# Performance work log

Hardware: AMD Instinct MI355X
Metric: run time of the kernel (lower is better)

Reference implementation:

```python
import jax, jax.numpy as jnp
import numpy as np

N = 50000      # nodes
E = 800000     # edges
DIN = 128
DH = 128
DE = 128
DOUT = 2
EPS = 1e-5     # GraphNorm eps


def _xavier(key, fan_in, fan_out):
    lim = float(np.sqrt(6.0 / (fan_in + fan_out)))
    return jax.random.uniform(key, (fan_in, fan_out), jnp.float32, -lim, lim)


def setup_inputs() -> dict:
    key = jax.random.key(0)
    ks = jax.random.split(key, 8)
    x = jax.random.normal(ks[0], (N, DIN), jnp.float32)
    edge_index = jax.random.randint(ks[1], (2, E), 0, N, dtype=jnp.int32)
    W1 = _xavier(ks[2], DIN, DH); b1 = jnp.zeros((DH,), jnp.float32)
    W2 = _xavier(ks[3], DH, DH);  b2 = jnp.zeros((DH,), jnp.float32)
    W3 = _xavier(ks[4], DH, DE);  b3 = jnp.zeros((DE,), jnp.float32)
    gn1_w = jnp.ones((DH,), jnp.float32); gn1_b = jnp.zeros((DH,), jnp.float32); gn1_a = jnp.ones((DH,), jnp.float32)
    gn2_w = jnp.ones((DH,), jnp.float32); gn2_b = jnp.zeros((DH,), jnp.float32); gn2_a = jnp.ones((DH,), jnp.float32)
    Wout = _xavier(ks[5], DE, DOUT); bout = jnp.zeros((DOUT,), jnp.float32)
    return {
        "x": x, "edge_index": edge_index,
        "W1": W1, "b1": b1, "W2": W2, "b2": b2, "W3": W3, "b3": b3,
        "gn1_w": gn1_w, "gn1_b": gn1_b, "gn1_a": gn1_a,
        "gn2_w": gn2_w, "gn2_b": gn2_b, "gn2_a": gn2_a,
        "Wout": Wout, "bout": bout,
    }


def gcn_conv(x, src, dst, W, b):
    # PyG GCNConv: add self-loops, symmetric normalization, linear, scatter-add at dst.
    n = x.shape[0]
    h = x @ W                                   # [N, C]
    loop = jnp.arange(n, dtype=src.dtype)
    s = jnp.concatenate([src, loop])            # [E+N]
    d = jnp.concatenate([dst, loop])
    deg = jnp.zeros((n,), h.dtype).at[d].add(1.0)
    dinv = jnp.where(deg > 0, jax.lax.rsqrt(deg), 0.0)
    norm = dinv[s] * dinv[d]                    # [E+N]
    out = jnp.zeros_like(h).at[d].add(h[s] * norm[:, None])
    return out + b


def graph_norm(h, w, b, alpha):
    # Single-graph GraphNorm: shift by alpha*mean, normalize by variance of shifted values.
    mean = h.mean(axis=0)
    c = h - alpha * mean
    var = (c * c).mean(axis=0)
    return c * jax.lax.rsqrt(var + EPS) * w + b


def reference(x, edge_index, W1, b1, W2, b2, W3, b3,
              gn1_w, gn1_b, gn1_a, gn2_w, gn2_b, gn2_a, Wout, bout):
    src, dst = edge_index[0], edge_index[1]
    h = gcn_conv(x, src, dst, W1, b1)
    h = jax.nn.relu(graph_norm(h, gn1_w, gn1_b, gn1_a))   # dropout identity (eval)
    h = gcn_conv(h, src, dst, W2, b2)
    h = jax.nn.relu(graph_norm(h, gn2_w, gn2_b, gn2_a))
    h = gcn_conv(h, src, dst, W3, b3)
    return h @ Wout + bout
```

## Files before the change

kernel.cpp:

```cpp
#include <hip/hip_runtime.h>
#include <hip/hip_bf16.h>

#define GN_EPS 1e-5f


typedef __attribute__((ext_vector_type(8))) short short8;
typedef __attribute__((ext_vector_type(4))) float f32x4;

__device__ __forceinline__ unsigned short f2bf(float f) {
    unsigned u = __float_as_uint(f);
    u += 0x7fffu + ((u >> 16) & 1u);
    return (unsigned short)(u >> 16);
}
__device__ __forceinline__ float bflo(unsigned u) { return __uint_as_float(u << 16); }
__device__ __forceinline__ float bfhi(unsigned u) { return __uint_as_float(u & 0xffff0000u); }

__global__ void k_degi(const int* __restrict__ dst, int* __restrict__ degi,
                       unsigned short* __restrict__ slot, int e) {
    int i = blockIdx.x * blockDim.x + threadIdx.x;
    if (i < e) slot[i] = (unsigned short)atomicAdd(&degi[dst[i]], 1);
}

#define SCAN_CHUNK 4096
__global__ __launch_bounds__(256) void k_blocksum(const int* __restrict__ degi,
                                                  int* __restrict__ partial, int n) {
    int base = blockIdx.x * SCAN_CHUNK + threadIdx.x * 16;
    int s = 0;
    #pragma unroll
    for (int q = 0; q < 16; ++q) {
        int i = base + q;
        if (i < n) s += degi[i];
    }
    #pragma unroll
    for (int off = 32; off; off >>= 1) s += __shfl_down(s, off);
    __shared__ int ws[4];
    if ((threadIdx.x & 63) == 0) ws[threadIdx.x >> 6] = s;
    __syncthreads();
    if (threadIdx.x == 0) partial[blockIdx.x] = ws[0] + ws[1] + ws[2] + ws[3];
}

__global__ __launch_bounds__(256) void k_scanfinal(const int* __restrict__ degi,
                                                   const int* __restrict__ partial,
                                                   int* __restrict__ rowptr,
                                                   float* __restrict__ dinv, int n, int nb) {
    int blockbase = 0;
    for (int i = 0; i < (int)blockIdx.x; ++i) blockbase += partial[i];

    int base = blockIdx.x * SCAN_CHUNK + threadIdx.x * 16;
    int v[16];
    int s = 0;
    #pragma unroll
    for (int q = 0; q < 16; ++q) {
        int i = base + q;
        v[q] = (i < n) ? degi[i] : 0;
        s += v[q];
    }
    const int lane = threadIdx.x & 63;
    const int wid = threadIdx.x >> 6;
    int x = s;
    #pragma unroll
    for (int off = 1; off < 64; off <<= 1) {
        int t = __shfl_up(x, off);
        if (lane >= off) x += t;
    }
    __shared__ int ws[4];
    if (lane == 63) ws[wid] = x;
    __syncthreads();
    int waveoff = 0;
    if (wid > 0) waveoff += ws[0];
    if (wid > 1) waveoff += ws[1];
    if (wid > 2) waveoff += ws[2];
    int excl = x - s + waveoff + blockbase;
    #pragma unroll
    for (int q = 0; q < 16; ++q) {
        int i = base + q;
        if (i < n) {
            rowptr[i] = excl;
            dinv[i] = rsqrtf((float)(v[q] + 1));
        }
        excl += v[q];
    }
    if ((int)blockIdx.x == nb - 1 && threadIdx.x == 255) {
        rowptr[n] = excl;
    }
}

__global__ void k_fill(const int* __restrict__ src, const int* __restrict__ dst,
                       const unsigned short* __restrict__ slot, const int* __restrict__ rowptr,
                       const float* __restrict__ dinv,
                       unsigned* __restrict__ csr_ew, int e) {
    int i = blockIdx.x * blockDim.x + threadIdx.x;
    if (i < e) {
        int s = src[i], d = dst[i];
        float w = dinv[s] * dinv[d];
        csr_ew[rowptr[d] + (int)slot[i]] = ((unsigned)s << 16) | (unsigned)f2bf(w);
    }
}

__global__ __launch_bounds__(256) void k_prepW2(const float* __restrict__ W1,
                                                const float* __restrict__ W2,
                                                unsigned short* __restrict__ Wt) {
    const float* W = blockIdx.x == 0 ? W1 : W2;
    unsigned short* o = Wt + blockIdx.x * 16384;
    __shared__ unsigned short sT[128 * 130];
    const float4* W4 = (const float4*)W;
    for (int idx = threadIdx.x; idx < 128 * 32; idx += 256) {
        int k = idx >> 5, c4 = idx & 31;
        float4 v = W4[k * 32 + c4];
        sT[(c4 * 4 + 0) * 130 + k] = f2bf(v.x);
        sT[(c4 * 4 + 1) * 130 + k] = f2bf(v.y);
        sT[(c4 * 4 + 2) * 130 + k] = f2bf(v.z);
        sT[(c4 * 4 + 3) * 130 + k] = f2bf(v.w);
    }
    __syncthreads();
    for (int idx = threadIdx.x; idx < 128 * 128; idx += 256) {
        int c = idx >> 7, k = idx & 127;
        o[idx] = sT[c * 130 + k];
    }
}

__global__ __launch_bounds__(128) void k_prepM(const float* __restrict__ W3,
                                               const float* __restrict__ Wo,
                                               const float* __restrict__ b3,
                                               const float* __restrict__ bo,
                                               float* __restrict__ M,
                                               float* __restrict__ mb) {
    int k = threadIdx.x;
    float m0 = 0.f, m1 = 0.f;
    for (int c = 0; c < 128; ++c) {
        float w = W3[k * 128 + c];
        m0 += w * Wo[c * 2];
        m1 += w * Wo[c * 2 + 1];
    }
    M[k * 2] = m0;
    M[k * 2 + 1] = m1;
    if (k < 2) {
        float s = 0.f;
        for (int c = 0; c < 128; ++c) s += b3[c] * Wo[c * 2 + k];
        mb[k] = s + bo[k];
    }
}

#define LDK 136
__global__ __launch_bounds__(256) void k_gemm_f32(const float* __restrict__ X,
                                                  const unsigned short* __restrict__ Wt,
                                                  unsigned short* __restrict__ Y,
                                                  int nrows) {
    __shared__ __align__(16) unsigned short sX[64 * LDK];
    __shared__ __align__(16) unsigned short sB[128 * LDK];
    const int t = threadIdx.x;
    const int row0 = blockIdx.x * 64;

    for (int idx = t; idx < 128 * 16; idx += 256) {
        int c = idx >> 4, ch = idx & 15;
        uint4 v = ((const uint4*)(Wt + c * 128))[ch];
        *(uint4*)(&sB[c * LDK + ch * 8]) = v;
    }
    for (int idx = t; idx < 64 * 32; idx += 256) {
        int r = idx >> 5, c4 = idx & 31;
        int grow = row0 + r;
        float4 v = make_float4(0.f, 0.f, 0.f, 0.f);
        if (grow < nrows) v = ((const float4*)(X + (size_t)grow * 128))[c4];
        ushort4 o;
        o.x = f2bf(v.x); o.y = f2bf(v.y); o.z = f2bf(v.z); o.w = f2bf(v.w);
        *(ushort4*)(&sX[r * LDK + c4 * 4]) = o;
    }
    __syncthreads();

    const int w = t >> 6;
    const int lane = t & 63;
    const int m = lane & 15;
    const int quad = lane >> 4;

    f32x4 acc[8] = {};
    #pragma unroll
    for (int ks = 0; ks < 4; ++ks) {
        int ko = ks * 32 + quad * 8;
        short8 a = *(const short8*)(&sX[(w * 16 + m) * LDK + ko]);
        #pragma unroll
        for (int ct = 0; ct < 8; ++ct) {
            short8 b = *(const short8*)(&sB[(ct * 16 + m) * LDK + ko]);
            acc[ct] = __builtin_amdgcn_mfma_f32_16x16x32_bf16(a, b, acc[ct], 0, 0, 0);
        }
    }
    #pragma unroll
    for (int r = 0; r < 4; ++r) {
        int grow = row0 + w * 16 + quad * 4 + r;
        if (grow >= nrows) continue;
        unsigned short* yr = Y + (size_t)grow * 128 + m;
        #pragma unroll
        for (int ct = 0; ct < 8; ++ct) yr[ct * 16] = f2bf(acc[ct][r]);
    }
}

__global__ __launch_bounds__(256) void k_gemm_bf(const unsigned short* __restrict__ Xb,
                                                 const unsigned short* __restrict__ Wt,
                                                 unsigned short* __restrict__ Y,
                                                 const float* __restrict__ cs,
                                                 const float* __restrict__ cb,
                                                 int nrows) {
    __shared__ __align__(16) unsigned short sX[64 * LDK];
    __shared__ __align__(16) unsigned short sB[128 * LDK];
    const int t = threadIdx.x;
    const int row0 = blockIdx.x * 64;

    for (int idx = t; idx < 128 * 16; idx += 256) {
        int c = idx >> 4, ch = idx & 15;
        uint4 v = ((const uint4*)(Wt + c * 128))[ch];
        *(uint4*)(&sB[c * LDK + ch * 8]) = v;
    }
    for (int idx = t; idx < 64 * 32; idx += 256) {
        int r = idx >> 5, c4 = idx & 31;
        int grow = row0 + r;
        uint2 u = make_uint2(0u, 0u);
        if (grow < nrows) u = *(const uint2*)(Xb + (size_t)grow * 128 + c4 * 4);
        float4 s4 = ((const float4*)cs)[c4];
        float4 b4 = ((const float4*)cb)[c4];
        ushort4 o;
        o.x = f2bf(fmaxf(fmaf(bflo(u.x), s4.x, b4.x), 0.f));
        o.y = f2bf(fmaxf(fmaf(bfhi(u.x), s4.y, b4.y), 0.f));
        o.z = f2bf(fmaxf(fmaf(bflo(u.y), s4.z, b4.z), 0.f));
        o.w = f2bf(fmaxf(fmaf(bfhi(u.y), s4.w, b4.w), 0.f));
        *(ushort4*)(&sX[r * LDK + c4 * 4]) = o;
    }
    __syncthreads();

    const int w = t >> 6;
    const int lane = t & 63;
    const int m = lane & 15;
    const int quad = lane >> 4;

    f32x4 acc[8] = {};
    #pragma unroll
    for (int ks = 0; ks < 4; ++ks) {
        int ko = ks * 32 + quad * 8;
        short8 a = *(const short8*)(&sX[(w * 16 + m) * LDK + ko]);
        #pragma unroll
        for (int ct = 0; ct < 8; ++ct) {
            short8 b = *(const short8*)(&sB[(ct * 16 + m) * LDK + ko]);
            acc[ct] = __builtin_amdgcn_mfma_f32_16x16x32_bf16(a, b, acc[ct], 0, 0, 0);
        }
    }
    #pragma unroll
    for (int r = 0; r < 4; ++r) {
        int grow = row0 + w * 16 + quad * 4 + r;
        if (grow >= nrows) continue;
        unsigned short* yr = Y + (size_t)grow * 128 + m;
        #pragma unroll
        for (int ct = 0; ct < 8; ++ct) yr[ct * 16] = f2bf(acc[ct][r]);
    }
}

__global__ __launch_bounds__(256) void k_gather(const unsigned short* __restrict__ H,
                                                unsigned short* __restrict__ O,
                                                const int* __restrict__ rowptr,
                                                const unsigned* __restrict__ csr_ew,
                                                const float* __restrict__ dinv,
                                                const float* __restrict__ bias, int n) {
    int node = blockIdx.x * 4 + (threadIdx.x >> 6);
    if (node >= n) return;
    int lane = threadIdx.x & 63;
    int qw = lane >> 4;
    int ql = lane & 15;
    const uint4* Hx = (const uint4*)H;
    float di = dinv[node];
    float acc[8] = {};
    if (qw == 0) {
        uint4 u = Hx[(size_t)node * 16 + ql];
        float dd = di * di;
        float4 ba = ((const float4*)bias)[ql * 2];
        float4 bb = ((const float4*)bias)[ql * 2 + 1];
        acc[0] = bflo(u.x) * dd + ba.x; acc[1] = bfhi(u.x) * dd + ba.y;
        acc[2] = bflo(u.y) * dd + ba.z; acc[3] = bfhi(u.y) * dd + ba.w;
        acc[4] = bflo(u.z) * dd + bb.x; acc[5] = bfhi(u.z) * dd + bb.y;
        acc[6] = bflo(u.w) * dd + bb.z; acc[7] = bfhi(u.w) * dd + bb.w;
    }
    int j = rowptr[node];
    const int end = rowptr[node + 1];
    for (; j + 15 < end; j += 16) {
        unsigned ew[4];
        #pragma unroll
        for (int q = 0; q < 4; ++q) ew[q] = csr_ew[j + 4 * q + qw];
        uint4 u[4];
        #pragma unroll
        for (int q = 0; q < 4; ++q) u[q] = Hx[(size_t)(ew[q] >> 16) * 16 + ql];
        #pragma unroll
        for (int q = 0; q < 4; ++q) {
            float nr = __uint_as_float(ew[q] << 16);
            acc[0] += bflo(u[q].x) * nr; acc[1] += bfhi(u[q].x) * nr;
            acc[2] += bflo(u[q].y) * nr; acc[3] += bfhi(u[q].y) * nr;
            acc[4] += bflo(u[q].z) * nr; acc[5] += bfhi(u[q].z) * nr;
            acc[6] += bflo(u[q].w) * nr; acc[7] += bfhi(u[q].w) * nr;
        }
    }
    for (int jj = j + qw; jj < end; jj += 4) {
        unsigned ew = csr_ew[jj];
        uint4 u = Hx[(size_t)(ew >> 16) * 16 + ql];
        float nr = __uint_as_float(ew << 16);
        acc[0] += bflo(u.x) * nr; acc[1] += bfhi(u.x) * nr;
        acc[2] += bflo(u.y) * nr; acc[3] += bfhi(u.y) * nr;
        acc[4] += bflo(u.z) * nr; acc[5] += bfhi(u.z) * nr;
        acc[6] += bflo(u.w) * nr; acc[7] += bfhi(u.w) * nr;
    }
    #pragma unroll
    for (int i = 0; i < 8; ++i) {
        acc[i] += __shfl_down(acc[i], 32);
        acc[i] += __shfl_down(acc[i], 16);
    }
    if (qw == 0) {
        uint4 o;
        o.x = (unsigned)f2bf(acc[0]) | ((unsigned)f2bf(acc[1]) << 16);
        o.y = (unsigned)f2bf(acc[2]) | ((unsigned)f2bf(acc[3]) << 16);
        o.z = (unsigned)f2bf(acc[4]) | ((unsigned)f2bf(acc[5]) << 16);
        o.w = (unsigned)f2bf(acc[6]) | ((unsigned)f2bf(acc[7]) << 16);
        *(uint4*)(O + (size_t)node * 128 + ql * 8) = o;
    }
}

__global__ __launch_bounds__(256) void k_zproj(const unsigned short* __restrict__ Xb,
                                               const float* __restrict__ M,
                                               const float* __restrict__ cs,
                                               const float* __restrict__ cb,
                                               float2* __restrict__ Z, int n) {
    int node = blockIdx.x * 4 + (threadIdx.x >> 6);
    if (node >= n) return;
    int lane = threadIdx.x & 63;
    unsigned u = ((const unsigned*)Xb)[(size_t)node * 64 + lane];
    int c0 = lane * 2;
    float a = fmaxf(fmaf(bflo(u), cs[c0], cb[c0]), 0.f);
    float b = fmaxf(fmaf(bfhi(u), cs[c0 + 1], cb[c0 + 1]), 0.f);
    float p0 = a * M[c0 * 2]     + b * M[(c0 + 1) * 2];
    float p1 = a * M[c0 * 2 + 1] + b * M[(c0 + 1) * 2 + 1];
    #pragma unroll
    for (int off = 32; off; off >>= 1) {
        p0 += __shfl_down(p0, off);
        p1 += __shfl_down(p1, off);
    }
    if (lane == 0) Z[node] = make_float2(p0, p1);
}

__global__ __launch_bounds__(256) void k_gatherZ(const float2* __restrict__ Z,
                                                 const int* __restrict__ rowptr,
                                                 const unsigned* __restrict__ csr_ew,
                                                 const float* __restrict__ dinv,
                                                 const float* __restrict__ mb,
                                                 float* __restrict__ out, int n) {
    int wid = threadIdx.x >> 6;
    int lane = threadIdx.x & 63;
    int g = lane >> 4;
    int gl = lane & 15;
    int node = blockIdx.x * 16 + wid * 4 + g;
    if (node >= n) return;
    float2 acc = make_float2(0.f, 0.f);
    if (gl == 0) {
        float di = dinv[node];
        float2 z = Z[node];
        acc.x = z.x * di * di + mb[0];
        acc.y = z.y * di * di + mb[1];
    }
    int j = rowptr[node];
    const int end = rowptr[node + 1];
    for (int jj = j + gl; jj < end; jj += 16) {
        unsigned ew = csr_ew[jj];
        float2 z = Z[ew >> 16];
        float w = __uint_as_float(ew << 16);
        acc.x += z.x * w;
        acc.y += z.y * w;
    }
    #pragma unroll
    for (int off = 8; off; off >>= 1) {
        acc.x += __shfl_down(acc.x, off);
        acc.y += __shfl_down(acc.y, off);
    }
    if (gl == 0) {
        out[(size_t)node * 2]     = acc.x;
        out[(size_t)node * 2 + 1] = acc.y;
    }
}

#define STAT_NB 256
__global__ __launch_bounds__(256) void k_stats(const unsigned short* __restrict__ H,
                                               float* __restrict__ pS,
                                               float* __restrict__ pQ, int n) {
    const uint4* H4 = (const uint4*)H;
    const size_t nv = (size_t)n * 16;
    float s[8] = {}, q[8] = {};
    for (size_t f = (size_t)blockIdx.x * 256 + threadIdx.x; f < nv;
         f += (size_t)256 * STAT_NB) {
        uint4 u = H4[f];
        float v;
        v = bflo(u.x); s[0] += v; q[0] += v * v;
        v = bfhi(u.x); s[1] += v; q[1] += v * v;
        v = bflo(u.y); s[2] += v; q[2] += v * v;
        v = bfhi(u.y); s[3] += v; q[3] += v * v;
        v = bflo(u.z); s[4] += v; q[4] += v * v;
        v = bfhi(u.z); s[5] += v; q[5] += v * v;
        v = bflo(u.w); s[6] += v; q[6] += v * v;
        v = bfhi(u.w); s[7] += v; q[7] += v * v;
    }
    __shared__ float ls[256][9], lq[256][9];
    int t = threadIdx.x;
    #pragma unroll
    for (int i = 0; i < 8; ++i) { ls[t][i] = s[i]; lq[t][i] = q[i]; }
    __syncthreads();
    #pragma unroll
    for (int off = 128; off >= 16; off >>= 1) {
        if (t < off) {
            #pragma unroll
            for (int i = 0; i < 8; ++i) { ls[t][i] += ls[t + off][i]; lq[t][i] += lq[t + off][i]; }
        }
        __syncthreads();
    }
    if (t < 16) {
        #pragma unroll
        for (int i = 0; i < 8; ++i) {
            pS[(size_t)blockIdx.x * 128 + t * 8 + i] = ls[t][i];
            pQ[(size_t)blockIdx.x * 128 + t * 8 + i] = lq[t][i];
        }
    }
}

__global__ void k_finstats(const float* __restrict__ pS, const float* __restrict__ pQ,
                           const float* __restrict__ w, const float* __restrict__ b,
                           const float* __restrict__ alpha,
                           float* __restrict__ colscale, float* __restrict__ colshift,
                           int n) {
    int c = threadIdx.x;
    if (c >= 128) return;
    float s = 0.f, q = 0.f;
    #pragma unroll 8
    for (int blk = 0; blk < STAT_NB; ++blk) {
        s += pS[blk * 128 + c];
        q += pQ[blk * 128 + c];
    }
    float inv_n = 1.0f / (float)n;
    float m = s * inv_n;
    float eh2 = q * inv_n;
    float a = alpha[c];
    float var = eh2 - (2.0f * a - a * a) * m * m;
    float scale = rsqrtf(var + GN_EPS) * w[c];
    colscale[c] = scale;
    colshift[c] = b[c] - a * m * scale;
}

extern "C" void kernel_launch(void* const* d_in, const int* in_sizes, int n_in,
                              void* d_out, int out_size, void* d_ws, size_t ws_size,
                              hipStream_t stream) {
    const float* x    = (const float*)d_in[0];
    const int*   ei   = (const int*)  d_in[1];
    const float* W1   = (const float*)d_in[2];
    const float* b1   = (const float*)d_in[3];
    const float* W2   = (const float*)d_in[4];
    const float* b2   = (const float*)d_in[5];
    const float* W3   = (const float*)d_in[6];
    const float* b3   = (const float*)d_in[7];
    const float* gn1w = (const float*)d_in[8];
    const float* gn1b = (const float*)d_in[9];
    const float* gn1a = (const float*)d_in[10];
    const float* gn2w = (const float*)d_in[11];
    const float* gn2b = (const float*)d_in[12];
    const float* gn2a = (const float*)d_in[13];
    const float* Wout = (const float*)d_in[14];
    const float* bout = (const float*)d_in[15];
    float* out = (float*)d_out;

    const int n = in_sizes[0] / 128;
    const int e = in_sizes[1] / 2;
    const int* srcI = ei;
    const int* dstI = ei + e;

    unsigned short* bufH = (unsigned short*)d_ws;
    unsigned short* bufG = bufH + (size_t)n * 128;
    unsigned short* slot = bufH;
    float* dinv     = (float*)(bufG + (size_t)n * 128);
    float* colscale = dinv + n;
    float* colshift = colscale + 128;
    int*   degi     = (int*)(colshift + 128);
    int*   rowptr   = degi + n;
    int*   partial  = rowptr + n + 1;
    float* pS       = (float*)(partial + 64);
    float* pQ       = pS + STAT_NB * 128;
    unsigned* csr_ew = (unsigned*)(pQ + STAT_NB * 128);
    unsigned short* Wt = (unsigned short*)(csr_ew + e);
    float* M        = (float*)(Wt + 2 * 16384);
    float* mb       = M + 256;
    float2* Z       = (float2*)(mb + 2);

    const int nb = (n + SCAN_CHUNK - 1) / SCAN_CHUNK;

    hipMemsetAsync(degi, 0, (size_t)n * sizeof(int), stream);
    k_degi<<<(e + 255) / 256, 256, 0, stream>>>(dstI, degi, slot, e);
    k_blocksum<<<nb, 256, 0, stream>>>(degi, partial, n);
    k_scanfinal<<<nb, 256, 0, stream>>>(degi, partial, rowptr, dinv, n, nb);
    k_fill<<<(e + 255) / 256, 256, 0, stream>>>(srcI, dstI, slot, rowptr, dinv, csr_ew, e);
    k_prepW2<<<2, 256, 0, stream>>>(W1, W2, Wt);
    k_prepM<<<1, 128, 0, stream>>>(W3, Wout, b3, bout, M, mb);

    const int gemmGrid = (n + 63) / 64;
    const int gathGrid = (n + 3) / 4;

    k_gemm_f32<<<gemmGrid, 256, 0, stream>>>(x, Wt, bufH, n);
    k_gather<<<gathGrid, 256, 0, stream>>>(bufH, bufG, rowptr, csr_ew, dinv, b1, n);
    k_stats<<<STAT_NB, 256, 0, stream>>>(bufG, pS, pQ, n);
    k_finstats<<<1, 128, 0, stream>>>(pS, pQ, gn1w, gn1b, gn1a, colscale, colshift, n);

    k_gemm_bf<<<gemmGrid, 256, 0, stream>>>(bufG, Wt + 16384, bufH, colscale, colshift, n);
    k_gather<<<gathGrid, 256, 0, stream>>>(bufH, bufG, rowptr, csr_ew, dinv, b2, n);
    k_stats<<<STAT_NB, 256, 0, stream>>>(bufG, pS, pQ, n);
    k_finstats<<<1, 128, 0, stream>>>(pS, pQ, gn2w, gn2b, gn2a, colscale, colshift, n);

    k_zproj<<<gathGrid, 256, 0, stream>>>(bufG, M, colscale, colshift, Z, n);
    k_gatherZ<<<(n + 15) / 16, 256, 0, stream>>>(Z, rowptr, csr_ew, dinv, mb, out, n);
}
```

Baseline: 317.2 us.

## Pad CSR rows to 16 and fuse GraphNorm stats into gather

```diff
diff --git a/kernel.cpp b/kernel.cpp
--- a/kernel.cpp
+++ b/kernel.cpp
@@ -1,5 +1,4 @@
 #include <hip/hip_runtime.h>
-#include <hip/hip_bf16.h>
 
 #define GN_EPS 1e-5f
 
@@ -29,7 +28,7 @@
     #pragma unroll
     for (int q = 0; q < 16; ++q) {
         int i = base + q;
-        if (i < n) s += degi[i];
+        if (i < n) s += (degi[i] + 15) & ~15;
     }
     #pragma unroll
     for (int off = 32; off; off >>= 1) s += __shfl_down(s, off);
@@ -47,13 +46,14 @@
     for (int i = 0; i < (int)blockIdx.x; ++i) blockbase += partial[i];
 
     int base = blockIdx.x * SCAN_CHUNK + threadIdx.x * 16;
-    int v[16];
+    int v[16], pv[16];
     int s = 0;
     #pragma unroll
     for (int q = 0; q < 16; ++q) {
         int i = base + q;
         v[q] = (i < n) ? degi[i] : 0;
-        s += v[q];
+        pv[q] = (v[q] + 15) & ~15;
+        s += pv[q];
     }
     const int lane = threadIdx.x & 63;
     const int wid = threadIdx.x >> 6;
@@ -78,7 +78,7 @@
             rowptr[i] = excl;
             dinv[i] = rsqrtf((float)(v[q] + 1));
         }
-        excl += v[q];
+        excl += pv[q];
     }
     if ((int)blockIdx.x == nb - 1 && threadIdx.x == 255) {
         rowptr[n] = excl;
@@ -97,47 +97,50 @@
     }
 }
 
-__global__ __launch_bounds__(256) void k_prepW2(const float* __restrict__ W1,
-                                                const float* __restrict__ W2,
-                                                unsigned short* __restrict__ Wt) {
-    const float* W = blockIdx.x == 0 ? W1 : W2;
-    unsigned short* o = Wt + blockIdx.x * 16384;
+__global__ __launch_bounds__(256) void k_prep(const float* __restrict__ W1,
+                                              const float* __restrict__ W2,
+                                              const float* __restrict__ W3,
+                                              const float* __restrict__ Wo,
+                                              const float* __restrict__ b3,
+                                              const float* __restrict__ bo,
+                                              unsigned short* __restrict__ Wt,
+                                              float* __restrict__ M,
+                                              float* __restrict__ mb) {
     __shared__ unsigned short sT[128 * 130];
-    const float4* W4 = (const float4*)W;
-    for (int idx = threadIdx.x; idx < 128 * 32; idx += 256) {
-        int k = idx >> 5, c4 = idx & 31;
-        float4 v = W4[k * 32 + c4];
-        sT[(c4 * 4 + 0) * 130 + k] = f2bf(v.x);
-        sT[(c4 * 4 + 1) * 130 + k] = f2bf(v.y);
-        sT[(c4 * 4 + 2) * 130 + k] = f2bf(v.z);
-        sT[(c4 * 4 + 3) * 130 + k] = f2bf(v.w);
-    }
-    __syncthreads();
-    for (int idx = threadIdx.x; idx < 128 * 128; idx += 256) {
-        int c = idx >> 7, k = idx & 127;
-        o[idx] = sT[c * 130 + k];
-    }
-}
-
-__global__ __launch_bounds__(128) void k_prepM(const float* __restrict__ W3,
-                                               const float* __restrict__ Wo,
-                                               const float* __restrict__ b3,
-                                               const float* __restrict__ bo,
-                                               float* __restrict__ M,
-                                               float* __restrict__ mb) {
-    int k = threadIdx.x;
-    float m0 = 0.f, m1 = 0.f;
-    for (int c = 0; c < 128; ++c) {
-        float w = W3[k * 128 + c];
-        m0 += w * Wo[c * 2];
-        m1 += w * Wo[c * 2 + 1];
-    }
-    M[k * 2] = m0;
-    M[k * 2 + 1] = m1;
-    if (k < 2) {
-        float s = 0.f;
-        for (int c = 0; c < 128; ++c) s += b3[c] * Wo[c * 2 + k];
-        mb[k] = s + bo[k];
+    if (blockIdx.x < 2) {
+        const float* W = blockIdx.x == 0 ? W1 : W2;
+        unsigned short* o = Wt + blockIdx.x * 16384;
+        const float4* W4 = (const float4*)W;
+        for (int idx = threadIdx.x; idx < 128 * 32; idx += 256) {
+            int k = idx >> 5, c4 = idx & 31;
+            float4 v = W4[k * 32 + c4];
+            sT[(c4 * 4 + 0) * 130 + k] = f2bf(v.x);
+            sT[(c4 * 4 + 1) * 130 + k] = f2bf(v.y);
+            sT[(c4 * 4 + 2) * 130 + k] = f2bf(v.z);
+            sT[(c4 * 4 + 3) * 130 + k] = f2bf(v.w);
+        }
+        __syncthreads();
+        for (int idx = threadIdx.x; idx < 128 * 128; idx += 256) {
+            int c = idx >> 7, k = idx & 127;
+            o[idx] = sT[c * 130 + k];
+        }
+    } else {
+        int k = threadIdx.x;
+        if (k < 128) {
+            float m0 = 0.f, m1 = 0.f;
+            for (int c = 0; c < 128; ++c) {
+                float w = W3[k * 128 + c];
+                m0 += w * Wo[c * 2];
+                m1 += w * Wo[c * 2 + 1];
+            }
+            M[k * 2] = m0;
+            M[k * 2 + 1] = m1;
+            if (k < 2) {
+                float s = 0.f;
+                for (int c = 0; c < 128; ++c) s += b3[c] * Wo[c * 2 + k];
+                mb[k] = s + bo[k];
+            }
+        }
     }
 }
 
@@ -256,64 +259,90 @@
                                                 const int* __restrict__ rowptr,
                                                 const unsigned* __restrict__ csr_ew,
                                                 const float* __restrict__ dinv,
-                                                const float* __restrict__ bias, int n) {
-    int node = blockIdx.x * 4 + (threadIdx.x >> 6);
-    if (node >= n) return;
-    int lane = threadIdx.x & 63;
-    int qw = lane >> 4;
-    int ql = lane & 15;
+                                                const float* __restrict__ bias,
+                                                float* __restrict__ pS,
+                                                float* __restrict__ pQ, int n) {
+    __shared__ float sS[4][128];
+    __shared__ float sQ[4][128];
+    const int wid = threadIdx.x >> 6;
+    const int node = blockIdx.x * 4 + wid;
+    const int lane = threadIdx.x & 63;
+    const int qw = lane >> 4;
+    const int ql = lane & 15;
     const uint4* Hx = (const uint4*)H;
-    float di = dinv[node];
     float acc[8] = {};
+    if (node < n) {
+        float di = dinv[node];
+        if (qw == 0) {
+            uint4 u = Hx[(size_t)node * 16 + ql];
+            float dd = di * di;
+            float4 ba = ((const float4*)bias)[ql * 2];
+            float4 bb = ((const float4*)bias)[ql * 2 + 1];
+            acc[0] = bflo(u.x) * dd + ba.x; acc[1] = bfhi(u.x) * dd + ba.y;
+            acc[2] = bflo(u.y) * dd + ba.z; acc[3] = bfhi(u.y) * dd + ba.w;
+            acc[4] = bflo(u.z) * dd + bb.x; acc[5] = bfhi(u.z) * dd + bb.y;
+            acc[6] = bflo(u.w) * dd + bb.z; acc[7] = bfhi(u.w) * dd + bb.w;
+        }
+        int j = rowptr[node];
+        const int end = rowptr[node + 1];
+        for (; j < end; j += 16) {
+            unsigned ew[4];
+            #pragma unroll
+            for (int q = 0; q < 4; ++q) ew[q] = csr_ew[j + 4 * q + qw];
+            uint4 u[4];
+            #pragma unroll
+            for (int q = 0; q < 4; ++q) {
+                unsigned idx = ((ew[q] >> 12) & 0xFFFF0u) + (unsigned)ql;
+                u[q] = Hx[idx];
+            }
+            #pragma unroll
+            for (int q = 0; q < 4; ++q) {
+                float nr = __uint_as_float(ew[q] << 16);
+                acc[0] += bflo(u[q].x) * nr; acc[1] += bfhi(u[q].x) * nr;
+                acc[2] += bflo(u[q].y) * nr; acc[3] += bfhi(u[q].y) * nr;
+                acc[4] += bflo(u[q].z) * nr; acc[5] += bfhi(u[q].z) * nr;
+                acc[6] += bflo(u[q].w) * nr; acc[7] += bfhi(u[q].w) * nr;
+            }
+        }
+        #pragma unroll
+        for (int i = 0; i < 8; ++i) {
+            acc[i] += __shfl_down(acc[i], 32);
+            acc[i] += __shfl_down(acc[i], 16);
+        }
+    }
     if (qw == 0) {
-        uint4 u = Hx[(size_t)node * 16 + ql];
-        float dd = di * di;
-        float4 ba = ((const float4*)bias)[ql * 2];
-        float4 bb = ((const float4*)bias)[ql * 2 + 1];
-        acc[0] = bflo(u.x) * dd + ba.x; acc[1] = bfhi(u.x) * dd + ba.y;
-        acc[2] = bflo(u.y) * dd + ba.z; acc[3] = bfhi(u.y) * dd + ba.w;
-        acc[4] = bflo(u.z) * dd + bb.x; acc[5] = bfhi(u.z) * dd + bb.y;
-        acc[6] = bflo(u.w) * dd + bb.z; acc[7] = bfhi(u.w) * dd + bb.w;
-    }
-    int j = rowptr[node];
-    const int end = rowptr[node + 1];
-    for (; j + 15 < end; j += 16) {
-        unsigned ew[4];
-        #pragma unroll
-        for (int q = 0; q < 4; ++q) ew[q] = csr_ew[j + 4 * q + qw];
-        uint4 u[4];
-        #pragma unroll
-        for (int q = 0; q < 4; ++q) u[q] = Hx[(size_t)(ew[q] >> 16) * 16 + ql];
-        #pragma unroll
-        for (int q = 0; q < 4; ++q) {
-            float nr = __uint_as_float(ew[q] << 16);
-            acc[0] += bflo(u[q].x) * nr; acc[1] += bfhi(u[q].x) * nr;
-            acc[2] += bflo(u[q].y) * nr; acc[3] += bfhi(u[q].y) * nr;
-            acc[4] += bflo(u[q].z) * nr; acc[5] += bfhi(u[q].z) * nr;
-            acc[6] += bflo(u[q].w) * nr; acc[7] += bfhi(u[q].w) * nr;
-        }
-    }
-    for (int jj = j + qw; jj < end; jj += 4) {
-        unsigned ew = csr_ew[jj];
-        uint4 u = Hx[(size_t)(ew >> 16) * 16 + ql];
-        float nr = __uint_as_float(ew << 16);
-        acc[0] += bflo(u.x) * nr; acc[1] += bfhi(u.x) * nr;
-        acc[2] += bflo(u.y) * nr; acc[3] += bfhi(u.y) * nr;
-        acc[4] += bflo(u.z) * nr; acc[5] += bfhi(u.z) * nr;
-        acc[6] += bflo(u.w) * nr; acc[7] += bfhi(u.w) * nr;
-    }
-    #pragma unroll
-    for (int i = 0; i < 8; ++i) {
-        acc[i] += __shfl_down(acc[i], 32);
-        acc[i] += __shfl_down(acc[i], 16);
-    }
-    if (qw == 0) {
-        uint4 o;
-        o.x = (unsigned)f2bf(acc[0]) | ((unsigned)f2bf(acc[1]) << 16);
-        o.y = (unsigned)f2bf(acc[2]) | ((unsigned)f2bf(acc[3]) << 16);
-        o.z = (unsigned)f2bf(acc[4]) | ((unsigned)f2bf(acc[5]) << 16);
-        o.w = (unsigned)f2bf(acc[6]) | ((unsigned)f2bf(acc[7]) << 16);
-        *(uint4*)(O + (size_t)node * 128 + ql * 8) = o;
+        if (node < n) {
+            unsigned short h[8];
+            float v[8];
+            #pragma unroll
+            for (int i = 0; i < 8; ++i) {
+                h[i] = f2bf(acc[i]);
+                v[i] = __uint_as_float((unsigned)h[i] << 16);
+                sS[wid][ql * 8 + i] = v[i];
+                sQ[wid][ql * 8 + i] = v[i] * v[i];
+            }
+            uint4 o;
+            o.x = (unsigned)h[0] | ((unsigned)h[1] << 16);
+            o.y = (unsigned)h[2] | ((unsigned)h[3] << 16);
+            o.z = (unsigned)h[4] | ((unsigned)h[5] << 16);
+            o.w = (unsigned)h[6] | ((unsigned)h[7] << 16);
+            *(uint4*)(O + (size_t)node * 128 + ql * 8) = o;
+        } else {
+            #pragma unroll
+            for (int i = 0; i < 8; ++i) {
+                sS[wid][ql * 8 + i] = 0.f;
+                sQ[wid][ql * 8 + i] = 0.f;
+            }
+        }
+    }
+    __syncthreads();
+    const int t = threadIdx.x;
+    if (t < 128) {
+        float s = sS[0][t] + sS[1][t] + sS[2][t] + sS[3][t];
+        float q = sQ[0][t] + sQ[1][t] + sQ[2][t] + sQ[3][t];
+        const int slotb = (blockIdx.x & 63) << 7;
+        atomicAdd(&pS[slotb + t], s);
+        atomicAdd(&pQ[slotb + t], q);
     }
 }
 
@@ -378,48 +407,6 @@
     }
 }
 
-#define STAT_NB 256
-__global__ __launch_bounds__(256) void k_stats(const unsigned short* __restrict__ H,
-                                               float* __restrict__ pS,
-                                               float* __restrict__ pQ, int n) {
-    const uint4* H4 = (const uint4*)H;
-    const size_t nv = (size_t)n * 16;
-    float s[8] = {}, q[8] = {};
-    for (size_t f = (size_t)blockIdx.x * 256 + threadIdx.x; f < nv;
-         f += (size_t)256 * STAT_NB) {
-        uint4 u = H4[f];
-        float v;
-        v = bflo(u.x); s[0] += v; q[0] += v * v;
-        v = bfhi(u.x); s[1] += v; q[1] += v * v;
-        v = bflo(u.y); s[2] += v; q[2] += v * v;
-        v = bfhi(u.y); s[3] += v; q[3] += v * v;
-        v = bflo(u.z); s[4] += v; q[4] += v * v;
-        v = bfhi(u.z); s[5] += v; q[5] += v * v;
-        v = bflo(u.w); s[6] += v; q[6] += v * v;
-        v = bfhi(u.w); s[7] += v; q[7] += v * v;
-    }
-    __shared__ float ls[256][9], lq[256][9];
-    int t = threadIdx.x;
-    #pragma unroll
-    for (int i = 0; i < 8; ++i) { ls[t][i] = s[i]; lq[t][i] = q[i]; }
-    __syncthreads();
-    #pragma unroll
-    for (int off = 128; off >= 16; off >>= 1) {
-        if (t < off) {
-            #pragma unroll
-            for (int i = 0; i < 8; ++i) { ls[t][i] += ls[t + off][i]; lq[t][i] += lq[t + off][i]; }
-        }
-        __syncthreads();
-    }
-    if (t < 16) {
-        #pragma unroll
-        for (int i = 0; i < 8; ++i) {
-            pS[(size_t)blockIdx.x * 128 + t * 8 + i] = ls[t][i];
-            pQ[(size_t)blockIdx.x * 128 + t * 8 + i] = lq[t][i];
-        }
-    }
-}
-
 __global__ void k_finstats(const float* __restrict__ pS, const float* __restrict__ pQ,
                            const float* __restrict__ w, const float* __restrict__ b,
                            const float* __restrict__ alpha,
@@ -429,7 +416,7 @@
     if (c >= 128) return;
     float s = 0.f, q = 0.f;
     #pragma unroll 8
-    for (int blk = 0; blk < STAT_NB; ++blk) {
+    for (int blk = 0; blk < 64; ++blk) {
         s += pS[blk * 128 + c];
         q += pQ[blk * 128 + c];
     }
@@ -469,45 +456,54 @@
     const int* srcI = ei;
     const int* dstI = ei + e;
 
-    unsigned short* bufH = (unsigned short*)d_ws;
-    unsigned short* bufG = bufH + (size_t)n * 128;
+    char* base = (char*)d_ws;
+    size_t off = 0;
+    auto take = [&](size_t bytes) -> void* {
+        void* r = base + off;
+        off += (bytes + 15) & ~(size_t)15;
+        return r;
+    };
+    unsigned short* bufH = (unsigned short*)take((size_t)n * 256);
+    unsigned short* bufG = (unsigned short*)take((size_t)n * 256);
+    float* dinv     = (float*)take((size_t)n * 4);
+    float* colscale = (float*)take(128 * 4);
+    float* colshift = (float*)take(128 * 4);
+    int*   rowptr   = (int*)take(((size_t)n + 1) * 4);
+    int*   partial  = (int*)take(64 * 4);
+    unsigned short* Wt = (unsigned short*)take(2 * 16384 * 2);
+    float* M        = (float*)take(256 * 4);
+    float* mb       = (float*)take(2 * 4);
+    float2* Z       = (float2*)take((size_t)n * 8);
+    int*   degi     = (int*)take((size_t)n * 4);
+    float* pS       = (float*)take(2 * 64 * 128 * 4);
+    float* pQ       = (float*)take(2 * 64 * 128 * 4);
+    size_t csr_cap  = (size_t)e + 16 * (size_t)n;
+    unsigned* csr_ew = (unsigned*)take(csr_cap * 4);
+    size_t zbytes   = (size_t)((base + off) - (char*)degi);
+
     unsigned short* slot = bufH;
-    float* dinv     = (float*)(bufG + (size_t)n * 128);
-    float* colscale = dinv + n;
-    float* colshift = colscale + 128;
-    int*   degi     = (int*)(colshift + 128);
-    int*   rowptr   = degi + n;
-    int*   partial  = rowptr + n + 1;
-    float* pS       = (float*)(partial + 64);
-    float* pQ       = pS + STAT_NB * 128;
-    unsigned* csr_ew = (unsigned*)(pQ + STAT_NB * 128);
-    unsigned short* Wt = (unsigned short*)(csr_ew + e);
-    float* M        = (float*)(Wt + 2 * 16384);
-    float* mb       = M + 256;
-    float2* Z       = (float2*)(mb + 2);
 
     const int nb = (n + SCAN_CHUNK - 1) / SCAN_CHUNK;
 
-    hipMemsetAsync(degi, 0, (size_t)n * sizeof(int), stream);
+    hipMemsetAsync(degi, 0, zbytes, stream);
     k_degi<<<(e + 255) / 256, 256, 0, stream>>>(dstI, degi, slot, e);
     k_blocksum<<<nb, 256, 0, stream>>>(degi, partial, n);
     k_scanfinal<<<nb, 256, 0, stream>>>(degi, partial, rowptr, dinv, n, nb);
     k_fill<<<(e + 255) / 256, 256, 0, stream>>>(srcI, dstI, slot, rowptr, dinv, csr_ew, e);
-    k_prepW2<<<2, 256, 0, stream>>>(W1, W2, Wt);
-    k_prepM<<<1, 128, 0, stream>>>(W3, Wout, b3, bout, M, mb);
+    k_prep<<<3, 256, 0, stream>>>(W1, W2, W3, Wout, b3, bout, Wt, M, mb);
 
     const int gemmGrid = (n + 63) / 64;
     const int gathGrid = (n + 3) / 4;
 
     k_gemm_f32<<<gemmGrid, 256, 0, stream>>>(x, Wt, bufH, n);
-    k_gather<<<gathGrid, 256, 0, stream>>>(bufH, bufG, rowptr, csr_ew, dinv, b1, n);
-    k_stats<<<STAT_NB, 256, 0, stream>>>(bufG, pS, pQ, n);
+    k_gather<<<gathGrid, 256, 0, stream>>>(bufH, bufG, rowptr, csr_ew, dinv, b1, pS, pQ, n);
     k_finstats<<<1, 128, 0, stream>>>(pS, pQ, gn1w, gn1b, gn1a, colscale, colshift, n);
 
     k_gemm_bf<<<gemmGrid, 256, 0, stream>>>(bufG, Wt + 16384, bufH, colscale, colshift, n);
-    k_gather<<<gathGrid, 256, 0, stream>>>(bufH, bufG, rowptr, csr_ew, dinv, b2, n);
-    k_stats<<<STAT_NB, 256, 0, stream>>>(bufG, pS, pQ, n);
-    k_finstats<<<1, 128, 0, stream>>>(pS, pQ, gn2w, gn2b, gn2a, colscale, colshift, n);
+    k_gather<<<gathGrid, 256, 0, stream>>>(bufH, bufG, rowptr, csr_ew, dinv, b2,
+                                           pS + 8192, pQ + 8192, n);
+    k_finstats<<<1, 128, 0, stream>>>(pS + 8192, pQ + 8192, gn2w, gn2b, gn2a,
+                                      colscale, colshift, n);
 
     k_zproj<<<gathGrid, 256, 0, stream>>>(bufG, M, colscale, colshift, Z, n);
     k_gatherZ<<<(n + 15) / 16, 256, 0, stream>>>(Z, rowptr, csr_ew, dinv, mb, out, n);
```

New measurement: 289.8 us. 8.6% less time.
